# Kernel optimization log

Hardware: AMD Instinct MI355X
Metric: run time of the kernel (lower is better)

## Reference

```python
import jax, jax.numpy as jnp
import numpy as np

B, S, DIM = 1, 2048, 2048
N_HEAD, N_KV, HEAD_DIM, ROPE = 32, 8, 64, 32
KV_SIZE = N_KV * HEAD_DIM


def setup_inputs() -> dict:
    key = jax.random.key(0)
    k1, k2, k3 = jax.random.split(key, 3)
    x = jax.random.normal(k1, (B, S, DIM), dtype=jnp.float32)
    # torch Linear weights, stored as (in, out) for right-multiplication
    wqkv = jax.random.normal(k2, (DIM, (N_HEAD + 2 * N_KV) * HEAD_DIM), dtype=jnp.float32) * (DIM ** -0.5)
    wo = jax.random.normal(k3, (N_HEAD * HEAD_DIM, DIM), dtype=jnp.float32) * (DIM ** -0.5)
    # standard rotate-half RoPE tables over the first ROPE dims of each head
    theta = 1.0 / (10000.0 ** (np.arange(0, ROPE, 2, dtype=np.float32) / ROPE))  # (ROPE/2,)
    ang = np.arange(S, dtype=np.float32)[:, None] * theta[None, :]               # (S, ROPE/2)
    cos = jnp.asarray(np.concatenate([np.cos(ang), np.cos(ang)], axis=-1))[None]  # (1, S, ROPE)
    sin = jnp.asarray(np.concatenate([np.sin(ang), np.sin(ang)], axis=-1))[None]  # (1, S, ROPE)
    return {"x": x, "cos": cos, "sin": sin, "wqkv": wqkv, "wo": wo}


def _apply_rope(xr, cos, sin):
    # xr: (B, H, S, ROPE); cos/sin: (1, S, ROPE) -> broadcast as (1, 1, S, ROPE)
    half = xr.shape[-1] // 2
    x1, x2 = xr[..., :half], xr[..., half:]
    rotated = jnp.concatenate((-x2, x1), axis=-1)
    diff = xr.ndim - cos.ndim
    if diff > 0:
        new_shape = cos.shape[:1] + (1,) * diff + cos.shape[1:]
        cos = cos.reshape(new_shape)
        sin = sin.reshape(new_shape)
    return xr * cos + rotated * sin


def _rope_emb(x, cos, sin):
    # partial RoPE: only first ROPE dims of head_dim are rotated
    return jnp.concatenate((_apply_rope(x[..., :ROPE], cos, sin), x[..., ROPE:]), axis=-1)


def reference(x, cos, sin, wqkv, wo):
    bsz, seqlen, _ = x.shape
    qkv = x @ wqkv  # (B, S, (H + 2*KV)*D)
    q, k, v = jnp.split(qkv, [DIM, DIM + KV_SIZE], axis=-1)
    q = q.reshape(bsz, seqlen, N_HEAD, HEAD_DIM).transpose(0, 2, 1, 3)   # (B, H, S, D)
    k = k.reshape(bsz, seqlen, N_KV, HEAD_DIM).transpose(0, 2, 1, 3)     # (B, KV, S, D)
    v = v.reshape(bsz, seqlen, N_KV, HEAD_DIM).transpose(0, 2, 1, 3)
    q = _rope_emb(q, cos, sin)
    k = _rope_emb(k, cos, sin)

    scale = 1.0 / (HEAD_DIM ** 0.5)
    group = N_HEAD // N_KV
    qg = q.reshape(bsz, N_KV, group, seqlen, HEAD_DIM)
    # GQA attention without materializing expanded K/V
    scores = jnp.einsum('bkgsd,bktd->bkgst', qg, k) * scale  # (B, KV, G, S, S)
    causal = jnp.tril(jnp.ones((seqlen, seqlen), dtype=bool))
    scores = jnp.where(causal, scores, jnp.finfo(scores.dtype).min)
    probs = jax.nn.softmax(scores, axis=-1)
    out = jnp.einsum('bkgst,bktd->bkgsd', probs, v)  # (B, KV, G, S, D)
    out = out.reshape(bsz, N_HEAD, seqlen, HEAD_DIM).transpose(0, 2, 1, 3).reshape(bsz, seqlen, DIM)
    return out @ wo
```

## Files before the change

kernel.cpp:

```cpp
#include <hip/hip_runtime.h>
#include <hip/hip_bf16.h>
#include <stdint.h>

typedef float f32x4 __attribute__((ext_vector_type(4)));
typedef float f32x4v __attribute__((ext_vector_type(4)));
typedef __bf16 bf16x8 __attribute__((ext_vector_type(8)));
typedef __bf16 bf16x4 __attribute__((ext_vector_type(4)));
typedef __bf16 bf16x2 __attribute__((ext_vector_type(2)));
typedef unsigned int u32x4 __attribute__((ext_vector_type(4)));

#define LOG2E 1.44269504088896340736f
#define MFMA16(a, b, c) __builtin_amdgcn_mfma_f32_16x16x32_bf16((a), (b), (c), 0, 0, 0)

static __device__ __forceinline__ void gload_lds16(const void* g, void* l) {
  __builtin_amdgcn_global_load_lds(
      (const __attribute__((address_space(1))) unsigned int*)g,
      (__attribute__((address_space(3))) unsigned int*)l, 16, 0, 0);
}

static __device__ __forceinline__ uint32_t pk2(float lo, float hi) {
  bf16x2 v;
  v[0] = (__bf16)lo;
  v[1] = (__bf16)hi;
  return __builtin_bit_cast(uint32_t, v);
}

__global__ __launch_bounds__(256) void prep(const float* __restrict__ x,
                                            __bf16* __restrict__ xb,
                                            const float* __restrict__ wqkv,
                                            __bf16* __restrict__ wqkvT,
                                            const float* __restrict__ wo,
                                            __bf16* __restrict__ woT) {
  __shared__ float tile[64][65];
  int b = blockIdx.x;
  int t = threadIdx.x;
  if (b < 4096) {
    int i = b * 256 + t;
    f32x4v v = *(const f32x4v*)(x + (size_t)i * 4);
    bf16x4 o;
    o[0] = (__bf16)v[0]; o[1] = (__bf16)v[1]; o[2] = (__bf16)v[2]; o[3] = (__bf16)v[3];
    *(bf16x4*)(xb + (size_t)i * 4) = o;
    return;
  }
  const float* in;
  __bf16* out;
  int R, C, bx, by;
  if (b < 5632) {
    int bb = b - 4096;
    in = wqkv; out = wqkvT; R = 2048; C = 3072; bx = bb % 48; by = bb / 48;
  } else {
    int bb = b - 5632;
    in = wo; out = woT; R = 2048; C = 2048; bx = bb & 31; by = bb >> 5;
  }
  int tr = by * 64, tc = bx * 64;
  int r0 = t >> 4;
  int c4 = (t & 15) * 4;
#pragma unroll
  for (int i = 0; i < 4; ++i) {
    int r = r0 + i * 16;
    f32x4v v = *(const f32x4v*)(in + (size_t)(tr + r) * C + tc + c4);
    tile[r][c4 + 0] = v[0]; tile[r][c4 + 1] = v[1];
    tile[r][c4 + 2] = v[2]; tile[r][c4 + 3] = v[3];
  }
  __syncthreads();
#pragma unroll
  for (int i = 0; i < 4; ++i) {
    int r = r0 + i * 16;
    __bf16* o = out + (size_t)(tc + r) * R + tr + c4;
    bf16x4 ov;
    ov[0] = (__bf16)tile[c4 + 0][r]; ov[1] = (__bf16)tile[c4 + 1][r];
    ov[2] = (__bf16)tile[c4 + 2][r]; ov[3] = (__bf16)tile[c4 + 3][r];
    *(bf16x4*)o = ov;
  }
}

template <typename OutT>
__global__ __launch_bounds__(256) void gemm64(const __bf16* __restrict__ A,
                                              const __bf16* __restrict__ BT,
                                              OutT* __restrict__ C,
                                              int M, int N, int K) {
  __shared__ alignas(16) __bf16 As[2][128 * 64];
  __shared__ alignas(16) __bf16 Bs[2][64 * 64];
  int gx = gridDim.x;
  int l = blockIdx.y * gx + blockIdx.x;
  int cpx = gx >> 3;
  int xcd = l & 7, rr0 = l >> 3;
  int bn = xcd * cpx + rr0 % cpx;
  int bm = rr0 / cpx;
  int t = threadIdx.x;
  int lane = t & 63, w = t >> 6;
  int lmod = lane & 15, ldiv = lane >> 4;

  f32x4 acc[2][4] = {};

  int sr8 = lane >> 3;
  int sk = (lane & 7) ^ sr8;
  const __bf16* gaB[4];
  const __bf16* gbB[2];
#pragma unroll
  for (int c = 0; c < 4; ++c) {
    int rr = (w * 4 + c) * 8 + sr8;
    gaB[c] = A + (size_t)(bm * 128 + rr) * K + sk * 8;
  }
#pragma unroll
  for (int c = 0; c < 2; ++c) {
    int rr = (w * 2 + c) * 8 + sr8;
    gbB[c] = BT + (size_t)(bn * 64 + rr) * K + sk * 8;
  }

#define GSTAGE64(buf, k0)                                              \
  {                                                                    \
    _Pragma("unroll") for (int c = 0; c < 4; ++c)                      \
        gload_lds16(gaB[c] + (k0), &As[buf][(w * 4 + c) * 512]);       \
    _Pragma("unroll") for (int c = 0; c < 2; ++c)                      \
        gload_lds16(gbB[c] + (k0), &Bs[buf][(w * 2 + c) * 512]);       \
  }

  int ca = ldiv ^ (lmod & 7);
  int cb = (4 + ldiv) ^ (lmod & 7);

  int NT = K >> 6;
  GSTAGE64(0, 0);
  int cur = 0;
  for (int tt = 0; tt < NT; ++tt) {
    __syncthreads();
    if (tt + 1 < NT) GSTAGE64(cur ^ 1, (tt + 1) * 64);

    bf16x8 af[2][2], bfv[4][2];
#pragma unroll
    for (int i = 0; i < 2; ++i) {
      const __bf16* p = &As[cur][(w * 32 + i * 16 + lmod) * 64];
      af[i][0] = *(const bf16x8*)(p + ca * 8);
      af[i][1] = *(const bf16x8*)(p + cb * 8);
    }
#pragma unroll
    for (int j = 0; j < 4; ++j) {
      const __bf16* p = &Bs[cur][(j * 16 + lmod) * 64];
      bfv[j][0] = *(const bf16x8*)(p + ca * 8);
      bfv[j][1] = *(const bf16x8*)(p + cb * 8);
    }
    __builtin_amdgcn_s_setprio(1);
#pragma unroll
    for (int i = 0; i < 2; ++i)
#pragma unroll
      for (int j = 0; j < 4; ++j) {
        acc[i][j] = MFMA16(af[i][0], bfv[j][0], acc[i][j]);
        acc[i][j] = MFMA16(af[i][1], bfv[j][1], acc[i][j]);
      }
    __builtin_amdgcn_s_setprio(0);
    cur ^= 1;
  }

#pragma unroll
  for (int i = 0; i < 2; ++i) {
    int row0 = bm * 128 + w * 32 + i * 16 + ldiv * 4;
#pragma unroll
    for (int j = 0; j < 4; ++j) {
      int col = bn * 64 + j * 16 + lmod;
#pragma unroll
      for (int r = 0; r < 4; ++r)
        C[(size_t)(row0 + r) * N + col] = (OutT)acc[i][j][r];
    }
  }
}

__global__ __launch_bounds__(256) void rope_restruct(__bf16* __restrict__ qkv,
                                                     const float* __restrict__ cosb,
                                                     const float* __restrict__ sinb,
                                                     __bf16* __restrict__ Kr,
                                                     __bf16* __restrict__ Vt) {
  int st = blockIdx.x * 64;
  int kvh = blockIdx.y;
  int t = threadIdx.x;
  __shared__ alignas(16) __bf16 vtile[64][72];
  const float csq = 0.125f * LOG2E;

  int r = t >> 2;
  int q4 = t & 3;
  int s = st + r;
  const float* cp = cosb + (size_t)s * 32;
  const float* sp = sinb + (size_t)s * 32;

  float cf[32], sf[32];
#pragma unroll
  for (int c = 0; c < 8; ++c) {
    f32x4v cv = *(const f32x4v*)(cp + c * 4);
    f32x4v sv = *(const f32x4v*)(sp + c * 4);
#pragma unroll
    for (int j = 0; j < 4; ++j) { cf[c * 4 + j] = cv[j]; sf[c * 4 + j] = sv[j]; }
  }

  {
    __bf16* p = qkv + (size_t)s * 3072 + (kvh * 4 + q4) * 64;
    bf16x8 q[8];
#pragma unroll
    for (int c = 0; c < 8; ++c) q[c] = *(const bf16x8*)(p + c * 8);
    float xf[32];
#pragma unroll
    for (int c = 0; c < 4; ++c)
#pragma unroll
      for (int j = 0; j < 8; ++j) xf[c * 8 + j] = (float)q[c][j];
    bf16x8 o[8];
#pragma unroll
    for (int d = 0; d < 16; ++d) {
      float o1 = (xf[d] * cf[d] - xf[d + 16] * sf[d]) * csq;
      float o2 = (xf[d + 16] * cf[d + 16] + xf[d] * sf[d + 16]) * csq;
      o[d >> 3][d & 7] = (__bf16)o1;
      o[(d + 16) >> 3][d & 7] = (__bf16)o2;
    }
#pragma unroll
    for (int c = 4; c < 8; ++c)
#pragma unroll
      for (int j = 0; j < 8; ++j) o[c][j] = (__bf16)((float)q[c][j] * csq);
#pragma unroll
    for (int c = 0; c < 8; ++c) *(bf16x8*)(p + c * 8) = o[c];
  }
  {
    const __bf16* p = qkv + (size_t)s * 3072 + 2048 + kvh * 64;
    __bf16* ko = Kr + ((size_t)kvh * 2048 + s) * 64;
    if (q4 == 0) {
      bf16x8 a0 = *(const bf16x8*)p, a1 = *(const bf16x8*)(p + 8);
      bf16x8 b0 = *(const bf16x8*)(p + 16), b1 = *(const bf16x8*)(p + 24);
      bf16x8 o0, o1;
#pragma unroll
      for (int j = 0; j < 8; ++j) {
        o0[j] = (__bf16)((float)a0[j] * cf[j] - (float)b0[j] * sf[j]);
        o1[j] = (__bf16)((float)a1[j] * cf[8 + j] - (float)b1[j] * sf[8 + j]);
      }
      *(bf16x8*)ko = o0;
      *(bf16x8*)(ko + 8) = o1;
    } else if (q4 == 1) {
      bf16x8 a0 = *(const bf16x8*)p, a1 = *(const bf16x8*)(p + 8);
      bf16x8 b0 = *(const bf16x8*)(p + 16), b1 = *(const bf16x8*)(p + 24);
      bf16x8 o0, o1;
#pragma unroll
      for (int j = 0; j < 8; ++j) {
        o0[j] = (__bf16)((float)b0[j] * cf[16 + j] + (float)a0[j] * sf[16 + j]);
        o1[j] = (__bf16)((float)b1[j] * cf[24 + j] + (float)a1[j] * sf[24 + j]);
      }
      *(bf16x8*)(ko + 16) = o0;
      *(bf16x8*)(ko + 24) = o1;
    } else if (q4 == 2) {
      *(bf16x8*)(ko + 32) = *(const bf16x8*)(p + 32);
      *(bf16x8*)(ko + 40) = *(const bf16x8*)(p + 40);
    } else {
      *(bf16x8*)(ko + 48) = *(const bf16x8*)(p + 48);
      *(bf16x8*)(ko + 56) = *(const bf16x8*)(p + 56);
    }
  }
  {
    const __bf16* p = qkv + (size_t)s * 3072 + 2560 + kvh * 64 + q4 * 16;
    *(bf16x8*)&vtile[r][q4 * 16] = *(const bf16x8*)p;
    *(bf16x8*)&vtile[r][q4 * 16 + 8] = *(const bf16x8*)(p + 8);
  }
  __syncthreads();
  {
    int d = t >> 2;
    __bf16* vo = Vt + ((size_t)kvh * 64 + d) * 2048 + st + q4 * 16;
#pragma unroll
    for (int j = 0; j < 16; ++j) vo[j] = vtile[q4 * 16 + j][d];
  }
}

__global__ __launch_bounds__(256) void attn_fwd(const __bf16* __restrict__ qkv,
                                                const __bf16* __restrict__ Kr,
                                                const __bf16* __restrict__ Vt,
                                                __bf16* __restrict__ O) {
  const int S = 2048, LDQ = 3072;
  int h = blockIdx.x;
  int b = blockIdx.y;
  int kvh = h >> 2;
  int t = threadIdx.x;
  int lane = t & 63, w = t >> 6;
  int lmod = lane & 15, ldiv = lane >> 4;

  __shared__ alignas(16) __bf16 KV[2][2][4096];

  const __bf16* Kg = Kr + (size_t)kvh * S * 64;
  const __bf16* Vg = Vt + (size_t)kvh * 64 * S;
  int srow8 = lane >> 3;
  int schk = (lane & 7) ^ srow8;

#define STAGE(buf, ks)                                                            \
  {                                                                               \
    __bf16* kb = &KV[buf][0][0];                                                  \
    __bf16* vb = &KV[buf][1][0];                                                  \
    _Pragma("unroll") for (int c = 0; c < 2; ++c) {                               \
      int c1kb = w * 2 + c;                                                       \
      int rr = c1kb * 8 + srow8;                                                  \
      int rrg = (rr & 0x23) | ((rr & 0x0C) << 1) | ((rr & 0x10) >> 2);            \
      gload_lds16(Kg + (size_t)((ks) + rrg) * 64 + schk * 8, kb + c1kb * 512);    \
      gload_lds16(Vg + (size_t)rr * S + (ks) + schk * 8, vb + c1kb * 512);        \
    }                                                                             \
  }

  int r7 = lmod & 7;
  int ca = ldiv ^ r7;
  int cb = (4 + ldiv) ^ r7;

#pragma unroll
  for (int seg = 0; seg < 2; ++seg) {
    int qt = seg ? (31 - b) : b;
    int nkt = qt + 1;
    int R0 = qt * 64 + w * 16;

    const __bf16* qp = qkv + (size_t)(R0 + lmod) * LDQ + h * 64 + ldiv * 8;
    bf16x8 qf0 = *(const bf16x8*)qp;
    bf16x8 qf1 = *(const bf16x8*)(qp + 32);

    f32x4 acc[4] = {};
    f32x4 lacc = {};

    __syncthreads();
    STAGE(0, 0);

    int cur = 0;
    for (int kt = 0; kt < nkt; ++kt) {
      int ks = kt * 64;
      __syncthreads();
      if (kt + 1 < nkt) STAGE(cur ^ 1, ks + 64);
      const __bf16* Ksb = &KV[cur][0][0];
      const __bf16* Vsb = &KV[cur][1][0];

      f32x4 st[4] = {};
      __builtin_amdgcn_s_setprio(1);
#pragma unroll
      for (int t16 = 0; t16 < 4; ++t16) {
        int row = t16 * 16 + lmod;
        bf16x8 kf0 = *(const bf16x8*)(Ksb + row * 64 + ca * 8);
        bf16x8 kf1 = *(const bf16x8*)(Ksb + row * 64 + cb * 8);
        st[t16] = MFMA16(kf0, qf0, st[t16]);
        st[t16] = MFMA16(kf1, qf1, st[t16]);
      }
      __builtin_amdgcn_s_setprio(0);

      if (kt == nkt - 1) {
        int qq = R0 + lmod;
#pragma unroll
        for (int t16 = 0; t16 < 4; ++t16) {
          int kk = ks + (t16 >> 1) * 32 + (t16 & 1) * 4 + ldiv * 8;
#pragma unroll
          for (int r = 0; r < 4; ++r)
            st[t16][r] = (kk + r) <= qq ? st[t16][r] : -1e30f;
        }
      }

      bf16x8 vf[8];
#pragma unroll
      for (int g2 = 0; g2 < 4; ++g2) {
        int row = g2 * 16 + lmod;
        vf[g2] = *(const bf16x8*)(Vsb + row * 64 + ca * 8);
        vf[4 + g2] = *(const bf16x8*)(Vsb + row * 64 + cb * 8);
      }

#pragma unroll
      for (int t16 = 0; t16 < 4; ++t16)
#pragma unroll
        for (int r = 0; r < 4; ++r) {
          float pv = __builtin_amdgcn_exp2f(st[t16][r]);
          st[t16][r] = pv;
          lacc[r] += pv;
        }

      u32x4 av0, av1;
      av0[0] = pk2(st[0][0], st[0][1]);
      av0[1] = pk2(st[0][2], st[0][3]);
      av0[2] = pk2(st[1][0], st[1][1]);
      av0[3] = pk2(st[1][2], st[1][3]);
      av1[0] = pk2(st[2][0], st[2][1]);
      av1[1] = pk2(st[2][2], st[2][3]);
      av1[2] = pk2(st[3][0], st[3][1]);
      av1[3] = pk2(st[3][2], st[3][3]);
      bf16x8 pa0 = __builtin_bit_cast(bf16x8, av0);
      bf16x8 pa1 = __builtin_bit_cast(bf16x8, av1);

      __builtin_amdgcn_s_setprio(1);
#pragma unroll
      for (int g2 = 0; g2 < 4; ++g2) {
        acc[g2] = MFMA16(pa0, vf[g2], acc[g2]);
        acc[g2] = MFMA16(pa1, vf[4 + g2], acc[g2]);
      }
      __builtin_amdgcn_s_setprio(0);
      cur ^= 1;
    }

    {
      float lsum = lacc[0] + lacc[1] + lacc[2] + lacc[3];
      lsum += __shfl_xor(lsum, 16);
      lsum += __shfl_xor(lsum, 32);
      float linv[4];
#pragma unroll
      for (int r = 0; r < 4; ++r) {
        float lq = __shfl(lsum, ldiv * 4 + r);
        linv[r] = 1.0f / lq;
      }
#pragma unroll
      for (int g2 = 0; g2 < 4; ++g2)
#pragma unroll
        for (int r = 0; r < 4; ++r)
          O[(size_t)(R0 + ldiv * 4 + r) * 2048 + h * 64 + g2 * 16 + lmod] =
              (__bf16)(acc[g2][r] * linv[r]);
    }
  }
}

extern "C" void kernel_launch(void* const* d_in, const int* in_sizes, int n_in,
                              void* d_out, int out_size, void* d_ws, size_t ws_size,
                              hipStream_t stream) {
  const float* x = (const float*)d_in[0];
  const float* cosb = (const float*)d_in[1];
  const float* sinb = (const float*)d_in[2];
  const float* wqkv = (const float*)d_in[3];
  const float* wo = (const float*)d_in[4];
  float* out = (float*)d_out;

  char* ws = (char*)d_ws;
  __bf16* xb    = (__bf16*)(ws + 0);
  __bf16* wqkvT = (__bf16*)(ws + 8388608);
  __bf16* woT   = (__bf16*)(ws + 20971520);
  __bf16* qkvb  = (__bf16*)(ws + 29360128);
  __bf16* Krb   = (__bf16*)(ws + 41943040);
  __bf16* Vtb   = (__bf16*)(ws + 44040192);
  __bf16* attnb = (__bf16*)(ws + 46137344);

  prep<<<6656, 256, 0, stream>>>(x, xb, wqkv, wqkvT, wo, woT);
  gemm64<__bf16><<<dim3(48, 16), 256, 0, stream>>>(xb, wqkvT, qkvb, 2048, 3072, 2048);
  rope_restruct<<<dim3(32, 8), 256, 0, stream>>>(qkvb, cosb, sinb, Krb, Vtb);
  attn_fwd<<<dim3(32, 16), 256, 0, stream>>>(qkvb, Krb, Vtb, attnb);
  gemm64<float><<<dim3(32, 16), 256, 0, stream>>>(attnb, woT, out, 2048, 2048, 2048);
}
```

Before: 113.9 us.

## Fuse RoPE, Q scaling, K layout and V transpose into QKV GEMM epilogue

Replaces the separate rope_restruct kernel with a dedicated QKV GEMM whose epilogue applies RoPE and the softmax scale to Q in place, writes rotated K into a per-head layout, and transposes V through LDS into Vt. This removes one kernel launch and a full read and rewrite of the QKV buffer. In exchange the epilogue does scalar scattered bf16 stores and reloads cos/sin per row, and the V tiles add extra LDS synchronization.

```diff
diff --git a/kernel.cpp b/kernel.cpp
--- a/kernel.cpp
+++ b/kernel.cpp
@@ -163,102 +163,134 @@
     }
   }
 }
-
-__global__ __launch_bounds__(256) void rope_restruct(__bf16* __restrict__ qkv,
-                                                     const float* __restrict__ cosb,
-                                                     const float* __restrict__ sinb,
-                                                     __bf16* __restrict__ Kr,
-                                                     __bf16* __restrict__ Vt) {
-  int st = blockIdx.x * 64;
-  int kvh = blockIdx.y;
+#undef GSTAGE64
+
+__global__ __launch_bounds__(256) void gemm_qkv(const __bf16* __restrict__ A,
+                                                const __bf16* __restrict__ BT,
+                                                __bf16* __restrict__ qkvb,
+                                                __bf16* __restrict__ Kr,
+                                                __bf16* __restrict__ Vt,
+                                                const float* __restrict__ cosb,
+                                                const float* __restrict__ sinb,
+                                                int M, int K) {
+  __shared__ alignas(16) __bf16 As[2][128 * 64];
+  __shared__ alignas(16) __bf16 Bs[2][64 * 64];
+  int gx = gridDim.x;
+  int l = blockIdx.y * gx + blockIdx.x;
+  int cpx = gx >> 3;
+  int xcd = l & 7, rr0 = l >> 3;
+  int bn = xcd * cpx + rr0 % cpx;
+  int bm = rr0 / cpx;
   int t = threadIdx.x;
-  __shared__ alignas(16) __bf16 vtile[64][72];
+  int lane = t & 63, w = t >> 6;
+  int lmod = lane & 15, ldiv = lane >> 4;
+
+  f32x4 acc[2][4] = {};
+
+  int sr8 = lane >> 3;
+  int sk = (lane & 7) ^ sr8;
+  const __bf16* gaB[4];
+  const __bf16* gbB[2];
+#pragma unroll
+  for (int c = 0; c < 4; ++c) {
+    int rr = (w * 4 + c) * 8 + sr8;
+    gaB[c] = A + (size_t)(bm * 128 + rr) * K + sk * 8;
+  }
+#pragma unroll
+  for (int c = 0; c < 2; ++c) {
+    int rr = (w * 2 + c) * 8 + sr8;
+    gbB[c] = BT + (size_t)(bn * 64 + rr) * K + sk * 8;
+  }
+
+#define GSTAGEQ(buf, k0)                                               \
+  {                                                                    \
+    _Pragma("unroll") for (int c = 0; c < 4; ++c)                      \
+        gload_lds16(gaB[c] + (k0), &As[buf][(w * 4 + c) * 512]);       \
+    _Pragma("unroll") for (int c = 0; c < 2; ++c)                      \
+        gload_lds16(gbB[c] + (k0), &Bs[buf][(w * 2 + c) * 512]);       \
+  }
+
+  int ca = ldiv ^ (lmod & 7);
+  int cb = (4 + ldiv) ^ (lmod & 7);
+
+  int NT = K >> 6;
+  GSTAGEQ(0, 0);
+  int cur = 0;
+  for (int tt = 0; tt < NT; ++tt) {
+    __syncthreads();
+    if (tt + 1 < NT) GSTAGEQ(cur ^ 1, (tt + 1) * 64);
+
+    bf16x8 af[2][2], bfv[4][2];
+#pragma unroll
+    for (int i = 0; i < 2; ++i) {
+      const __bf16* p = &As[cur][(w * 32 + i * 16 + lmod) * 64];
+      af[i][0] = *(const bf16x8*)(p + ca * 8);
+      af[i][1] = *(const bf16x8*)(p + cb * 8);
+    }
+#pragma unroll
+    for (int j = 0; j < 4; ++j) {
+      const __bf16* p = &Bs[cur][(j * 16 + lmod) * 64];
+      bfv[j][0] = *(const bf16x8*)(p + ca * 8);
+      bfv[j][1] = *(const bf16x8*)(p + cb * 8);
+    }
+    __builtin_amdgcn_s_setprio(1);
+#pragma unroll
+    for (int i = 0; i < 2; ++i)
+#pragma unroll
+      for (int j = 0; j < 4; ++j) {
+        acc[i][j] = MFMA16(af[i][0], bfv[j][0], acc[i][j]);
+        acc[i][j] = MFMA16(af[i][1], bfv[j][1], acc[i][j]);
+      }
+    __builtin_amdgcn_s_setprio(0);
+    cur ^= 1;
+  }
+#undef GSTAGEQ
+
   const float csq = 0.125f * LOG2E;
-
-  int r = t >> 2;
-  int q4 = t & 3;
-  int s = st + r;
-  const float* cp = cosb + (size_t)s * 32;
-  const float* sp = sinb + (size_t)s * 32;
-
-  float cf[32], sf[32];
-#pragma unroll
-  for (int c = 0; c < 8; ++c) {
-    f32x4v cv = *(const f32x4v*)(cp + c * 4);
-    f32x4v sv = *(const f32x4v*)(sp + c * 4);
-#pragma unroll
-    for (int j = 0; j < 4; ++j) { cf[c * 4 + j] = cv[j]; sf[c * 4 + j] = sv[j]; }
-  }
-
-  {
-    __bf16* p = qkv + (size_t)s * 3072 + (kvh * 4 + q4) * 64;
-    bf16x8 q[8];
-#pragma unroll
-    for (int c = 0; c < 8; ++c) q[c] = *(const bf16x8*)(p + c * 8);
-    float xf[32];
+  if (bn < 40) {
+    bool isQ = (bn < 32);
+    float sc = isQ ? csq : 1.0f;
+#pragma unroll
+    for (int i = 0; i < 2; ++i)
+#pragma unroll
+      for (int r = 0; r < 4; ++r) {
+        int s = bm * 128 + w * 32 + i * 16 + ldiv * 4 + r;
+        const float* cp = cosb + (size_t)s * 32;
+        const float* sp = sinb + (size_t)s * 32;
+        float c0 = cp[lmod], c1 = cp[16 + lmod];
+        float s0 = sp[lmod], s1 = sp[16 + lmod];
+        float a0 = acc[i][0][r], a1 = acc[i][1][r];
+        float o0 = (a0 * c0 - a1 * s0) * sc;
+        float o1 = (a1 * c1 + a0 * s1) * sc;
+        float o2 = acc[i][2][r] * sc;
+        float o3 = acc[i][3][r] * sc;
+        __bf16* dst = isQ ? (qkvb + (size_t)s * 3072 + bn * 64)
+                          : (Kr + ((size_t)(bn - 32) * 2048 + s) * 64);
+        dst[lmod] = (__bf16)o0;
+        dst[16 + lmod] = (__bf16)o1;
+        dst[32 + lmod] = (__bf16)o2;
+        dst[48 + lmod] = (__bf16)o3;
+      }
+  } else {
+    int kvh = bn - 40;
+    __bf16* tr = &As[0][0];
+    __syncthreads();
+#pragma unroll
+    for (int i = 0; i < 2; ++i)
+#pragma unroll
+      for (int j = 0; j < 4; ++j)
+#pragma unroll
+        for (int r = 0; r < 4; ++r)
+          tr[(j * 16 + lmod) * 136 + w * 32 + i * 16 + ldiv * 4 + r] =
+              (__bf16)acc[i][j][r];
+    __syncthreads();
+    int col = t >> 2;
+    int rseg = (t & 3) * 32;
+    const __bf16* src = tr + col * 136 + rseg;
+    __bf16* dst = Vt + ((size_t)kvh * 64 + col) * 2048 + bm * 128 + rseg;
 #pragma unroll
     for (int c = 0; c < 4; ++c)
-#pragma unroll
-      for (int j = 0; j < 8; ++j) xf[c * 8 + j] = (float)q[c][j];
-    bf16x8 o[8];
-#pragma unroll
-    for (int d = 0; d < 16; ++d) {
-      float o1 = (xf[d] * cf[d] - xf[d + 16] * sf[d]) * csq;
-      float o2 = (xf[d + 16] * cf[d + 16] + xf[d] * sf[d + 16]) * csq;
-      o[d >> 3][d & 7] = (__bf16)o1;
-      o[(d + 16) >> 3][d & 7] = (__bf16)o2;
-    }
-#pragma unroll
-    for (int c = 4; c < 8; ++c)
-#pragma unroll
-      for (int j = 0; j < 8; ++j) o[c][j] = (__bf16)((float)q[c][j] * csq);
-#pragma unroll
-    for (int c = 0; c < 8; ++c) *(bf16x8*)(p + c * 8) = o[c];
-  }
-  {
-    const __bf16* p = qkv + (size_t)s * 3072 + 2048 + kvh * 64;
-    __bf16* ko = Kr + ((size_t)kvh * 2048 + s) * 64;
-    if (q4 == 0) {
-      bf16x8 a0 = *(const bf16x8*)p, a1 = *(const bf16x8*)(p + 8);
-      bf16x8 b0 = *(const bf16x8*)(p + 16), b1 = *(const bf16x8*)(p + 24);
-      bf16x8 o0, o1;
-#pragma unroll
-      for (int j = 0; j < 8; ++j) {
-        o0[j] = (__bf16)((float)a0[j] * cf[j] - (float)b0[j] * sf[j]);
-        o1[j] = (__bf16)((float)a1[j] * cf[8 + j] - (float)b1[j] * sf[8 + j]);
-      }
-      *(bf16x8*)ko = o0;
-      *(bf16x8*)(ko + 8) = o1;
-    } else if (q4 == 1) {
-      bf16x8 a0 = *(const bf16x8*)p, a1 = *(const bf16x8*)(p + 8);
-      bf16x8 b0 = *(const bf16x8*)(p + 16), b1 = *(const bf16x8*)(p + 24);
-      bf16x8 o0, o1;
-#pragma unroll
-      for (int j = 0; j < 8; ++j) {
-        o0[j] = (__bf16)((float)b0[j] * cf[16 + j] + (float)a0[j] * sf[16 + j]);
-        o1[j] = (__bf16)((float)b1[j] * cf[24 + j] + (float)a1[j] * sf[24 + j]);
-      }
-      *(bf16x8*)(ko + 16) = o0;
-      *(bf16x8*)(ko + 24) = o1;
-    } else if (q4 == 2) {
-      *(bf16x8*)(ko + 32) = *(const bf16x8*)(p + 32);
-      *(bf16x8*)(ko + 40) = *(const bf16x8*)(p + 40);
-    } else {
-      *(bf16x8*)(ko + 48) = *(const bf16x8*)(p + 48);
-      *(bf16x8*)(ko + 56) = *(const bf16x8*)(p + 56);
-    }
-  }
-  {
-    const __bf16* p = qkv + (size_t)s * 3072 + 2560 + kvh * 64 + q4 * 16;
-    *(bf16x8*)&vtile[r][q4 * 16] = *(const bf16x8*)p;
-    *(bf16x8*)&vtile[r][q4 * 16 + 8] = *(const bf16x8*)(p + 8);
-  }
-  __syncthreads();
-  {
-    int d = t >> 2;
-    __bf16* vo = Vt + ((size_t)kvh * 64 + d) * 2048 + st + q4 * 16;
-#pragma unroll
-    for (int j = 0; j < 16; ++j) vo[j] = vtile[q4 * 16 + j][d];
+      *(bf16x8*)(dst + c * 8) = *(const bf16x8*)(src + c * 8);
   }
 }
 
@@ -424,8 +456,8 @@
   __bf16* attnb = (__bf16*)(ws + 46137344);
 
   prep<<<6656, 256, 0, stream>>>(x, xb, wqkv, wqkvT, wo, woT);
-  gemm64<__bf16><<<dim3(48, 16), 256, 0, stream>>>(xb, wqkvT, qkvb, 2048, 3072, 2048);
-  rope_restruct<<<dim3(32, 8), 256, 0, stream>>>(qkvb, cosb, sinb, Krb, Vtb);
+  gemm_qkv<<<dim3(48, 16), 256, 0, stream>>>(xb, wqkvT, qkvb, Krb, Vtb,
+                                             cosb, sinb, 2048, 2048);
   attn_fwd<<<dim3(32, 16), 256, 0, stream>>>(qkvb, Krb, Vtb, attnb);
   gemm64<float><<<dim3(32, 16), 256, 0, stream>>>(attnb, woT, out, 2048, 2048, 2048);
 }
```

New measurement: 107.0 us. -6.1%, faster.
